# Kernel tuning notes

Measured on AMD Instinct MI355X. Metric: run time of the kernel, lower is better.

The kernel has to match this reference:

```python
import jax, jax.numpy as jnp
import numpy as np

N, C, G, H = 262144, 512, 16, 16   # nodes, channels, groups, half_group_c
GH = G * H                          # 256
CH_HID = 64                         # channel_mlp hidden = max(GH//4, 8)
SP_HID = 8                          # space_mlp hidden = max(H//4, 8)
B = 1024                            # number of graphs
TEMP = 1.0
EPS = 1e-5


def setup_inputs() -> dict:
    k = jax.random.key(0)
    ks = jax.random.split(k, 20)
    s = 0.02
    rn = lambda kk, sh: jax.random.normal(kk, sh, dtype=jnp.float32)
    return {
        "x": rn(ks[0], (N, C)),
        "batch": jnp.sort(jax.random.randint(ks[1], (N,), 0, B, dtype=jnp.int32)),
        "num_segments": B,
        "cweight": s * rn(ks[2], (1, H)),
        "cbias": 1.0 + s * rn(ks[3], (1, H)),
        "sweight": s * rn(ks[4], (1, H)),
        "sbias": 1.0 + s * rn(ks[5], (1, H)),
        "ch_W1": rn(ks[6], (2 * GH, CH_HID)) / np.sqrt(2 * GH),
        "ch_b1": s * rn(ks[7], (CH_HID,)),
        "ch_W2": rn(ks[8], (CH_HID, GH)) / np.sqrt(CH_HID),
        "ch_b2": s * rn(ks[9], (GH,)),
        "gn_weight": 1.0 + s * rn(ks[10], (GH,)),
        "gn_bias": s * rn(ks[11], (GH,)),
        "sp_W1": rn(ks[12], (3 * H, SP_HID)) / np.sqrt(3 * H),
        "sp_b1": s * rn(ks[13], (SP_HID,)),
        "sp_W2": rn(ks[14], (SP_HID, H)) / np.sqrt(SP_HID),
        "sp_b2": s * rn(ks[15], (H,)),
        "init_scale": jnp.float32(0.1),
        "gnorm_weight": 1.0 + s * rn(ks[16], (C,)),
        "gnorm_bias": s * rn(ks[17], (C,)),
        "gnorm_mean_scale": 1.0 + s * rn(ks[18], (C,)),
    }


def reference(x, batch, num_segments, cweight, cbias, sweight, sbias,
              ch_W1, ch_b1, ch_W2, ch_b2, gn_weight, gn_bias,
              sp_W1, sp_b1, sp_W2, sp_b2, init_scale,
              gnorm_weight, gnorm_bias, gnorm_mean_scale):
    n = x.shape[0]
    xg = x.reshape(n, G, 2 * H)
    x_c = xg[:, :, :H]                      # [N, G, H] channel branch
    x_s = xg[:, :, H:]                      # [N, G, H] spatial branch
    xcf = x_c.reshape(n, GH)

    # --- segment mean / max pooling over graphs ---
    cnt = jax.ops.segment_sum(jnp.ones((n,), x.dtype), batch, num_segments)  # [B]
    gap_mean = jax.ops.segment_sum(xcf, batch, num_segments) / jnp.maximum(cnt, 1.0)[:, None]
    gap_max = jax.ops.segment_max(xcf, batch, num_segments)
    gap_max = jnp.where(cnt[:, None] > 0, gap_max, 0.0)    # empty graphs -> 0
    gap_cat = jnp.concatenate([gap_mean, gap_max], axis=1)  # [B, 2*GH]

    # --- channel gate MLP ---
    hch = jax.nn.relu(gap_cat @ ch_W1 + ch_b1)
    ch_gate = jax.nn.sigmoid((hch @ ch_W2 + ch_b2).reshape(-1, G, H) / TEMP)
    ch_gate = ch_gate * (1.0 + cweight.reshape(1, 1, H)) + cbias.reshape(1, 1, H)
    x_c = x_c * ch_gate[batch]

    # --- GroupNorm over each group's H channels (spatial extent 1) ---
    mu = x_s.mean(axis=2, keepdims=True)
    var = ((x_s - mu) ** 2).mean(axis=2, keepdims=True)
    xn = (x_s - mu) / jnp.sqrt(var + EPS)
    xn = xn * gn_weight.reshape(1, G, H) + gn_bias.reshape(1, G, H)

    # --- spatial context across groups (std is unbiased, ddof=1) ---
    mean_ctx = xn.mean(axis=1)
    max_ctx = xn.max(axis=1)
    std_ctx = jnp.sqrt(((xn - mean_ctx[:, None, :]) ** 2).sum(axis=1) / (G - 1))
    sc = jnp.concatenate([mean_ctx, max_ctx, std_ctx], axis=-1)  # [N, 3H]
    hs = jax.nn.relu(sc @ sp_W1 + sp_b1)
    sp_gate = jax.nn.sigmoid((hs @ sp_W2 + sp_b2).reshape(n, 1, H) / TEMP)
    sp_gate = sp_gate * (1.0 + sweight.reshape(1, 1, H)) + sbias.reshape(1, 1, H)
    x_s = x_s * sp_gate

    # stack -> [N,G,H,2] -> permute -> [N,G,2,H] -> [N,C]
    out = jnp.stack([x_c, x_s], axis=-1).transpose(0, 1, 3, 2).reshape(n, C)
    out = out + jnp.tanh(init_scale) * x

    # --- GraphNorm (PyG): per-graph, per-channel ---
    inv_cnt = 1.0 / jnp.maximum(cnt, 1.0)[:, None]
    gmean = jax.ops.segment_sum(out, batch, num_segments) * inv_cnt
    outc = out - gmean[batch] * gnorm_mean_scale
    gvar = jax.ops.segment_sum(outc * outc, batch, num_segments) * inv_cnt
    out = gnorm_weight * outc / jnp.sqrt(gvar + EPS)[batch] + gnorm_bias

    # channel shuffle with groups=2
    return out.reshape(n, 2, C // 2).transpose(0, 2, 1).reshape(n, C)
```

## Files before the change

### kernel.cpp

```cpp
#include <hip/hip_runtime.h>
#include <hip/hip_bf16.h>
#include <math.h>

#define NN 262144
#define CC 512
#define BB 1024
#define EPSF 1e-5f

typedef float f32x4 __attribute__((ext_vector_type(4)));

__device__ __forceinline__ int lower_bound_i(const int* __restrict__ a, int n, int v) {
    int lo = 0, hi = n;
    while (lo < hi) { int mid = (lo + hi) >> 1; if (a[mid] < v) lo = mid + 1; else hi = mid; }
    return lo;
}

__device__ __forceinline__ float sigmoidf(float v) { return 1.0f / (1.0f + __expf(-v)); }

template<int CTRL>
__device__ __forceinline__ float dppAdd(float v) {
    int t = __builtin_amdgcn_update_dpp(0, __float_as_int(v), CTRL, 0xf, 0xf, true);
    return v + __int_as_float(t);
}
template<int CTRL>
__device__ __forceinline__ float dppMax(float v) {
    int t = __builtin_amdgcn_update_dpp(0, __float_as_int(v), CTRL, 0xf, 0xf, true);
    return fmaxf(v, __int_as_float(t));
}

__global__ void kA(const float* __restrict__ x, const int* __restrict__ batch,
                   const float* __restrict__ sweight, const float* __restrict__ sbias,
                   const float* __restrict__ gn_w, const float* __restrict__ gn_b,
                   const float* __restrict__ sp_W1, const float* __restrict__ sp_b1,
                   const float* __restrict__ sp_W2, const float* __restrict__ sp_b2,
                   const float* __restrict__ init_scale,
                   float* __restrict__ segS1, float* __restrict__ segMx,
                   float* __restrict__ segS2, float* __restrict__ segT1,
                   float* __restrict__ segT2, int* __restrict__ segCnt,
                   float* __restrict__ spgt)
{
    const int b    = blockIdx.x;
    const int tid  = threadIdx.x;
    const int lane = tid & 63;
    const int w    = tid >> 6;
    const int g    = lane & 15;
    const int q    = lane >> 4;
    const int h0   = q * 4;
    const int kk   = g & 7;

    __shared__ float red[4][5][256];

    const int s = lower_bound_i(batch, NN, b);
    const int e = lower_bound_i(batch, NN, b + 1);
    const float tau = tanhf(init_scale[0]);

    float gwv[4], gbv[4], b2v[4], swv[4], sbv[4], w1m[4], w1x[4], w1s[4], w2r[4];
#pragma unroll
    for (int j = 0; j < 4; ++j) {
        const int h = h0 + j;
        gwv[j] = gn_w[g * 16 + h];
        gbv[j] = gn_b[g * 16 + h];
        b2v[j] = sp_b2[h];
        swv[j] = sweight[h];
        sbv[j] = sbias[h];
        w1m[j] = sp_W1[h * 8 + kk];
        w1x[j] = sp_W1[(16 + h) * 8 + kk];
        w1s[j] = sp_W1[(32 + h) * 8 + kk];
        w2r[j] = sp_W2[kk * 16 + h];
    }
    const float b1k = sp_b1[kk];

    float sc1[4] = {0.f,0.f,0.f,0.f}, sc2[4] = {0.f,0.f,0.f,0.f};
    float st1[4] = {0.f,0.f,0.f,0.f}, st2[4] = {0.f,0.f,0.f,0.f};
    float mxc[4] = {-INFINITY,-INFINITY,-INFINITY,-INFINITY};

    for (int n = s + w; n < e; n += 4) {
        const float* row = x + (size_t)n * CC + g * 32 + h0;
        const float4 c4 = *(const float4*)row;
        const float4 s4 = *(const float4*)(row + 16);
        float ca[4] = {c4.x, c4.y, c4.z, c4.w};
        float sa[4] = {s4.x, s4.y, s4.z, s4.w};

#pragma unroll
        for (int j = 0; j < 4; ++j) {
            sc1[j] += ca[j];
            sc2[j] = fmaf(ca[j], ca[j], sc2[j]);
            mxc[j] = fmaxf(mxc[j], ca[j]);
        }

        float ls = sa[0] + sa[1] + sa[2] + sa[3];
        float lq = fmaf(sa[0], sa[0], fmaf(sa[1], sa[1], fmaf(sa[2], sa[2], sa[3] * sa[3])));
        ls += __shfl_xor(ls, 16); ls += __shfl_xor(ls, 32);
        lq += __shfl_xor(lq, 16); lq += __shfl_xor(lq, 32);
        const float mu   = ls * 0.0625f;
        const float var  = lq * 0.0625f - mu * mu;
        const float rstd = rsqrtf(var + EPSF);
        float xn[4];
#pragma unroll
        for (int j = 0; j < 4; ++j)
            xn[j] = fmaf((sa[j] - mu) * rstd, gwv[j], gbv[j]);

        float sm[4], mx[4];
#pragma unroll
        for (int j = 0; j < 4; ++j) {
            float v = xn[j];
            v = dppAdd<0xB1>(v); v = dppAdd<0x4E>(v);
            v = dppAdd<0x124>(v); v = dppAdd<0x128>(v);
            sm[j] = v;
            float m = xn[j];
            m = dppMax<0xB1>(m); m = dppMax<0x4E>(m);
            m = dppMax<0x124>(m); m = dppMax<0x128>(m);
            mx[j] = m;
        }
        float mean[4], ssq[4];
#pragma unroll
        for (int j = 0; j < 4; ++j) {
            mean[j] = sm[j] * 0.0625f;
            const float d = xn[j] - mean[j];
            float v = d * d;
            v = dppAdd<0xB1>(v); v = dppAdd<0x4E>(v);
            v = dppAdd<0x124>(v); v = dppAdd<0x128>(v);
            ssq[j] = v;
        }
        float stdc[4];
#pragma unroll
        for (int j = 0; j < 4; ++j) stdc[j] = sqrtf(ssq[j] * (1.0f / 15.0f));

        float p = 0.f;
#pragma unroll
        for (int j = 0; j < 4; ++j) {
            p = fmaf(mean[j], w1m[j], p);
            p = fmaf(mx[j],   w1x[j], p);
            p = fmaf(stdc[j], w1s[j], p);
        }
        p += __shfl_xor(p, 16); p += __shfl_xor(p, 32);
        const float hsk = fmaxf(p + b1k, 0.0f);

        float spg[4];
#pragma unroll
        for (int j = 0; j < 4; ++j) {
            float t = hsk * w2r[j];
            t = dppAdd<0xB1>(t); t = dppAdd<0x4E>(t); t = dppAdd<0x141>(t);
            spg[j] = fmaf(sigmoidf(t + b2v[j]), 1.0f + swv[j], sbv[j]) + tau;
        }

#pragma unroll
        for (int j = 0; j < 4; ++j) {
            const float os = spg[j] * sa[j];
            st1[j] += os;
            st2[j] = fmaf(os, os, st2[j]);
        }

        if (g == 0) {
            *(float4*)(spgt + (size_t)n * 16 + h0) =
                make_float4(spg[0], spg[1], spg[2], spg[3]);
        }
    }

    const int ch = g * 16 + h0;
    *(float4*)&red[w][0][ch] = make_float4(sc1[0], sc1[1], sc1[2], sc1[3]);
    *(float4*)&red[w][1][ch] = make_float4(mxc[0], mxc[1], mxc[2], mxc[3]);
    *(float4*)&red[w][2][ch] = make_float4(sc2[0], sc2[1], sc2[2], sc2[3]);
    *(float4*)&red[w][3][ch] = make_float4(st1[0], st1[1], st1[2], st1[3]);
    *(float4*)&red[w][4][ch] = make_float4(st2[0], st2[1], st2[2], st2[3]);
    __syncthreads();
    if (tid < 256) {
        const int c = tid;
        float a0 = red[0][0][c] + red[1][0][c] + red[2][0][c] + red[3][0][c];
        float a1 = fmaxf(fmaxf(red[0][1][c], red[1][1][c]), fmaxf(red[2][1][c], red[3][1][c]));
        float a2 = red[0][2][c] + red[1][2][c] + red[2][2][c] + red[3][2][c];
        float a3 = red[0][3][c] + red[1][3][c] + red[2][3][c] + red[3][3][c];
        float a4 = red[0][4][c] + red[1][4][c] + red[2][4][c] + red[3][4][c];
        segS1[b * 256 + c] = a0;
        segMx[b * 256 + c] = a1;
        segS2[b * 256 + c] = a2;
        segT1[b * 256 + c] = a3;
        segT2[b * 256 + c] = a4;
    }
    if (tid == 0) segCnt[b] = e - s;
}

__global__ void kF(const float* __restrict__ segS1, const float* __restrict__ segMx,
                   const float* __restrict__ segS2, const float* __restrict__ segT1,
                   const float* __restrict__ segT2, const int* __restrict__ segCnt,
                   const float* __restrict__ ch_W1, const float* __restrict__ ch_b1,
                   const float* __restrict__ ch_W2, const float* __restrict__ ch_b2,
                   const float* __restrict__ cweight, const float* __restrict__ cbias,
                   const float* __restrict__ init_scale,
                   const float* __restrict__ gms, const float* __restrict__ gw,
                   const float* __restrict__ gb,
                   float* __restrict__ coef, float* __restrict__ offs)
{
    const int b = blockIdx.x;
    const int tid = threadIdx.x;
    __shared__ float gap[512];
    __shared__ float hch[64];
    __shared__ float part[4][64];

    const int cnt = segCnt[b];
    const float inv = 1.0f / (float)max(cnt, 1);
    if (tid < 256) {
        gap[tid] = segS1[b * 256 + tid] * inv;
        const float m = segMx[b * 256 + tid];
        gap[256 + tid] = (cnt > 0) ? m : 0.0f;
    }
    __syncthreads();
    {
        const int t = tid & 63, pp = tid >> 6;
        float acc = 0.f;
        for (int i = pp * 128; i < pp * 128 + 128; ++i)
            acc = fmaf(gap[i], ch_W1[i * 64 + t], acc);
        part[pp][t] = acc;
    }
    __syncthreads();
    if (tid < 64)
        hch[tid] = fmaxf(part[0][tid] + part[1][tid] + part[2][tid] + part[3][tid] + ch_b1[tid], 0.0f);
    __syncthreads();
    if (tid < 256) {
        const int c = tid, gg = c >> 4, h = c & 15;
        float acc = ch_b2[c];
        for (int k = 0; k < 64; ++k) acc = fmaf(hch[k], ch_W2[k * 256 + c], acc);
        const float chg = fmaf(sigmoidf(acc), 1.0f + cweight[h], cbias[h]);
        const float tau = tanhf(init_scale[0]);
        const float ct = chg + tau;
        const int colc = gg * 32 + h, cols = colc + 16;
        {
            const float S1 = segS1[b * 256 + c], S2 = segS2[b * 256 + c];
            const float m  = ct * S1 * inv;
            const float e2 = ct * ct * S2 * inv;
            const float smv = gms[colc];
            const float gv = fmaxf(e2 - m * m * smv * (2.0f - smv), 0.0f);
            const float A  = gw[colc] * rsqrtf(gv + EPSF);
            coef[b * 512 + colc] = A * ct;
            offs[b * 512 + colc] = gb[colc] - m * smv * A;
        }
        {
            const float T1 = segT1[b * 256 + c], T2 = segT2[b * 256 + c];
            const float m  = T1 * inv;
            const float e2 = T2 * inv;
            const float smv = gms[cols];
            const float gv = fmaxf(e2 - m * m * smv * (2.0f - smv), 0.0f);
            const float A  = gw[cols] * rsqrtf(gv + EPSF);
            coef[b * 512 + cols] = A;
            offs[b * 512 + cols] = gb[cols] - m * smv * A;
        }
    }
}

__global__ void kB(const float* __restrict__ x, const int* __restrict__ batch,
                   const float* __restrict__ coef, const float* __restrict__ offs,
                   const float* __restrict__ spgt, float* __restrict__ out)
{
    const int b = BB - 1 - blockIdx.x;
    const int tid = threadIdx.x;
    const int lane = tid & 63, w = tid >> 6;
    const int l2 = lane * 2;
    const int p0 = (lane >> 3) & 1;

    const int s = lower_bound_i(batch, NN, b);
    const int e = lower_bound_i(batch, NN, b + 1);

    const float* cfb = coef + (size_t)b * 512;
    const float* ofb = offs + (size_t)b * 512;
    const float cf0 = cfb[l2],       cf1 = cfb[l2 + 1];
    const float cf2 = cfb[128 + l2], cf3 = cfb[129 + l2];
    const float cf4 = cfb[256 + l2], cf5 = cfb[257 + l2];
    const float cf6 = cfb[384 + l2], cf7 = cfb[385 + l2];
    const float of0 = ofb[l2],       of1 = ofb[l2 + 1];
    const float of2 = ofb[128 + l2], of3 = ofb[129 + l2];
    const float of4 = ofb[256 + l2], of5 = ofb[257 + l2];
    const float of6 = ofb[384 + l2], of7 = ofb[385 + l2];

    for (int n = s + w; n < e; n += 4) {
        const float2* r2 = (const float2*)(x + (size_t)n * CC);
        const float2 xa = r2[lane];
        const float2 xb = r2[64 + lane];
        const float2 xc = r2[128 + lane];
        const float2 xd = r2[192 + lane];
        const float2 sp = *(const float2*)(spgt + (size_t)n * 16 + (l2 & 15));
        const float me = p0 ? sp.x : 1.0f;
        const float mo = p0 ? sp.y : 1.0f;

        const float v0 = fmaf(cf0 * me, xa.x, of0);
        const float v1 = fmaf(cf1 * mo, xa.y, of1);
        const float v2 = fmaf(cf2 * me, xb.x, of2);
        const float v3 = fmaf(cf3 * mo, xb.y, of3);
        const float v4 = fmaf(cf4 * me, xc.x, of4);
        const float v5 = fmaf(cf5 * mo, xc.y, of5);
        const float v6 = fmaf(cf6 * me, xd.x, of6);
        const float v7 = fmaf(cf7 * mo, xd.y, of7);

        f32x4* o4 = (f32x4*)(out + (size_t)n * CC);
        f32x4 pa = {v0, v4, v1, v5};
        f32x4 pb = {v2, v6, v3, v7};
        __builtin_nontemporal_store(pa, &o4[lane]);
        __builtin_nontemporal_store(pb, &o4[64 + lane]);
    }
}

extern "C" void kernel_launch(void* const* d_in, const int* in_sizes, int n_in,
                              void* d_out, int out_size, void* d_ws, size_t ws_size,
                              hipStream_t stream) {
    (void)in_sizes; (void)n_in; (void)out_size; (void)ws_size;
    const float* x        = (const float*)d_in[0];
    const int*   batch    = (const int*)d_in[1];
    const float* cweight  = (const float*)d_in[3];
    const float* cbias    = (const float*)d_in[4];
    const float* sweight  = (const float*)d_in[5];
    const float* sbias    = (const float*)d_in[6];
    const float* ch_W1    = (const float*)d_in[7];
    const float* ch_b1    = (const float*)d_in[8];
    const float* ch_W2    = (const float*)d_in[9];
    const float* ch_b2    = (const float*)d_in[10];
    const float* gn_w     = (const float*)d_in[11];
    const float* gn_b     = (const float*)d_in[12];
    const float* sp_W1    = (const float*)d_in[13];
    const float* sp_b1    = (const float*)d_in[14];
    const float* sp_W2    = (const float*)d_in[15];
    const float* sp_b2    = (const float*)d_in[16];
    const float* init_sc  = (const float*)d_in[17];
    const float* gnw      = (const float*)d_in[18];
    const float* gnb      = (const float*)d_in[19];
    const float* gms      = (const float*)d_in[20];

    float* ws    = (float*)d_ws;
    float* segS1 = ws;
    float* segMx = segS1 + BB * 256;
    float* segS2 = segMx + BB * 256;
    float* segT1 = segS2 + BB * 256;
    float* segT2 = segT1 + BB * 256;
    int*   segCnt = (int*)(segT2 + BB * 256);
    float* coef  = (float*)(segCnt + BB);
    float* offs  = coef + BB * 512;
    float* spgt  = offs + BB * 512;
    float* outp  = (float*)d_out;

    kA<<<BB, 256, 0, stream>>>(x, batch, sweight, sbias, gn_w, gn_b,
                               sp_W1, sp_b1, sp_W2, sp_b2, init_sc,
                               segS1, segMx, segS2, segT1, segT2, segCnt, spgt);
    kF<<<BB, 256, 0, stream>>>(segS1, segMx, segS2, segT1, segT2, segCnt,
                               ch_W1, ch_b1, ch_W2, ch_b2, cweight, cbias,
                               init_sc, gms, gnw, gnb, coef, offs);
    kB<<<BB, 256, 0, stream>>>(x, batch, coef, offs, spgt, outp);
}
```

Baseline: 484.0 us.

## Fuse pooling, gate MLP and GraphNorm apply into one per-graph kernel

```diff
diff --git a/kernel.cpp b/kernel.cpp
--- a/kernel.cpp
+++ b/kernel.cpp
@@ -6,6 +6,7 @@
 #define CC 512
 #define BB 1024
 #define EPSF 1e-5f
+#define CAP 512
 
 typedef float f32x4 __attribute__((ext_vector_type(4)));
 
@@ -28,18 +29,29 @@
     return fmaxf(v, __int_as_float(t));
 }
 
-__global__ void kA(const float* __restrict__ x, const int* __restrict__ batch,
-                   const float* __restrict__ sweight, const float* __restrict__ sbias,
-                   const float* __restrict__ gn_w, const float* __restrict__ gn_b,
-                   const float* __restrict__ sp_W1, const float* __restrict__ sp_b1,
-                   const float* __restrict__ sp_W2, const float* __restrict__ sp_b2,
-                   const float* __restrict__ init_scale,
-                   float* __restrict__ segS1, float* __restrict__ segMx,
-                   float* __restrict__ segS2, float* __restrict__ segT1,
-                   float* __restrict__ segT2, int* __restrict__ segCnt,
-                   float* __restrict__ spgt)
+__global__ __launch_bounds__(512, 1) void kFused(
+    const float* __restrict__ x, const int* __restrict__ batch,
+    const float* __restrict__ cweight, const float* __restrict__ cbias,
+    const float* __restrict__ sweight, const float* __restrict__ sbias,
+    const float* __restrict__ ch_W1, const float* __restrict__ ch_b1,
+    const float* __restrict__ ch_W2, const float* __restrict__ ch_b2,
+    const float* __restrict__ gn_w, const float* __restrict__ gn_b,
+    const float* __restrict__ sp_W1, const float* __restrict__ sp_b1,
+    const float* __restrict__ sp_W2, const float* __restrict__ sp_b2,
+    const float* __restrict__ init_scale,
+    const float* __restrict__ gms, const float* __restrict__ gw,
+    const float* __restrict__ gb,
+    float* __restrict__ spgOv, float* __restrict__ out)
 {
-    const int b    = blockIdx.x;
+    __shared__ float red[8][5][256];
+    __shared__ float segA[5][256];
+    __shared__ float spgL[CAP * 16];
+    __shared__ float gap[512];
+    __shared__ float part[8][64];
+    __shared__ float hch[64];
+    __shared__ float cA[512];
+    __shared__ float oA[512];
+
     const int tid  = threadIdx.x;
     const int lane = tid & 63;
     const int w    = tid >> 6;
@@ -47,11 +59,6 @@
     const int q    = lane >> 4;
     const int h0   = q * 4;
     const int kk   = g & 7;
-
-    __shared__ float red[4][5][256];
-
-    const int s = lower_bound_i(batch, NN, b);
-    const int e = lower_bound_i(batch, NN, b + 1);
     const float tau = tanhf(init_scale[0]);
 
     float gwv[4], gbv[4], b2v[4], swv[4], sbv[4], w1m[4], w1x[4], w1s[4], w2r[4];
@@ -70,231 +77,217 @@
     }
     const float b1k = sp_b1[kk];
 
-    float sc1[4] = {0.f,0.f,0.f,0.f}, sc2[4] = {0.f,0.f,0.f,0.f};
-    float st1[4] = {0.f,0.f,0.f,0.f}, st2[4] = {0.f,0.f,0.f,0.f};
-    float mxc[4] = {-INFINITY,-INFINITY,-INFINITY,-INFINITY};
-
-    for (int n = s + w; n < e; n += 4) {
-        const float* row = x + (size_t)n * CC + g * 32 + h0;
-        const float4 c4 = *(const float4*)row;
-        const float4 s4 = *(const float4*)(row + 16);
-        float ca[4] = {c4.x, c4.y, c4.z, c4.w};
-        float sa[4] = {s4.x, s4.y, s4.z, s4.w};
-
-#pragma unroll
-        for (int j = 0; j < 4; ++j) {
-            sc1[j] += ca[j];
-            sc2[j] = fmaf(ca[j], ca[j], sc2[j]);
-            mxc[j] = fmaxf(mxc[j], ca[j]);
-        }
-
-        float ls = sa[0] + sa[1] + sa[2] + sa[3];
-        float lq = fmaf(sa[0], sa[0], fmaf(sa[1], sa[1], fmaf(sa[2], sa[2], sa[3] * sa[3])));
-        ls += __shfl_xor(ls, 16); ls += __shfl_xor(ls, 32);
-        lq += __shfl_xor(lq, 16); lq += __shfl_xor(lq, 32);
-        const float mu   = ls * 0.0625f;
-        const float var  = lq * 0.0625f - mu * mu;
-        const float rstd = rsqrtf(var + EPSF);
-        float xn[4];
-#pragma unroll
-        for (int j = 0; j < 4; ++j)
-            xn[j] = fmaf((sa[j] - mu) * rstd, gwv[j], gbv[j]);
-
-        float sm[4], mx[4];
-#pragma unroll
-        for (int j = 0; j < 4; ++j) {
-            float v = xn[j];
-            v = dppAdd<0xB1>(v); v = dppAdd<0x4E>(v);
-            v = dppAdd<0x124>(v); v = dppAdd<0x128>(v);
-            sm[j] = v;
-            float m = xn[j];
-            m = dppMax<0xB1>(m); m = dppMax<0x4E>(m);
-            m = dppMax<0x124>(m); m = dppMax<0x128>(m);
-            mx[j] = m;
-        }
-        float mean[4], ssq[4];
-#pragma unroll
-        for (int j = 0; j < 4; ++j) {
-            mean[j] = sm[j] * 0.0625f;
-            const float d = xn[j] - mean[j];
-            float v = d * d;
-            v = dppAdd<0xB1>(v); v = dppAdd<0x4E>(v);
-            v = dppAdd<0x124>(v); v = dppAdd<0x128>(v);
-            ssq[j] = v;
-        }
-        float stdc[4];
-#pragma unroll
-        for (int j = 0; j < 4; ++j) stdc[j] = sqrtf(ssq[j] * (1.0f / 15.0f));
-
-        float p = 0.f;
-#pragma unroll
-        for (int j = 0; j < 4; ++j) {
-            p = fmaf(mean[j], w1m[j], p);
-            p = fmaf(mx[j],   w1x[j], p);
-            p = fmaf(stdc[j], w1s[j], p);
-        }
-        p += __shfl_xor(p, 16); p += __shfl_xor(p, 32);
-        const float hsk = fmaxf(p + b1k, 0.0f);
-
-        float spg[4];
-#pragma unroll
-        for (int j = 0; j < 4; ++j) {
-            float t = hsk * w2r[j];
-            t = dppAdd<0xB1>(t); t = dppAdd<0x4E>(t); t = dppAdd<0x141>(t);
-            spg[j] = fmaf(sigmoidf(t + b2v[j]), 1.0f + swv[j], sbv[j]) + tau;
-        }
-
-#pragma unroll
-        for (int j = 0; j < 4; ++j) {
-            const float os = spg[j] * sa[j];
-            st1[j] += os;
-            st2[j] = fmaf(os, os, st2[j]);
-        }
-
-        if (g == 0) {
-            *(float4*)(spgt + (size_t)n * 16 + h0) =
-                make_float4(spg[0], spg[1], spg[2], spg[3]);
-        }
-    }
-
-    const int ch = g * 16 + h0;
-    *(float4*)&red[w][0][ch] = make_float4(sc1[0], sc1[1], sc1[2], sc1[3]);
-    *(float4*)&red[w][1][ch] = make_float4(mxc[0], mxc[1], mxc[2], mxc[3]);
-    *(float4*)&red[w][2][ch] = make_float4(sc2[0], sc2[1], sc2[2], sc2[3]);
-    *(float4*)&red[w][3][ch] = make_float4(st1[0], st1[1], st1[2], st1[3]);
-    *(float4*)&red[w][4][ch] = make_float4(st2[0], st2[1], st2[2], st2[3]);
-    __syncthreads();
-    if (tid < 256) {
-        const int c = tid;
-        float a0 = red[0][0][c] + red[1][0][c] + red[2][0][c] + red[3][0][c];
-        float a1 = fmaxf(fmaxf(red[0][1][c], red[1][1][c]), fmaxf(red[2][1][c], red[3][1][c]));
-        float a2 = red[0][2][c] + red[1][2][c] + red[2][2][c] + red[3][2][c];
-        float a3 = red[0][3][c] + red[1][3][c] + red[2][3][c] + red[3][3][c];
-        float a4 = red[0][4][c] + red[1][4][c] + red[2][4][c] + red[3][4][c];
-        segS1[b * 256 + c] = a0;
-        segMx[b * 256 + c] = a1;
-        segS2[b * 256 + c] = a2;
-        segT1[b * 256 + c] = a3;
-        segT2[b * 256 + c] = a4;
-    }
-    if (tid == 0) segCnt[b] = e - s;
-}
-
-__global__ void kF(const float* __restrict__ segS1, const float* __restrict__ segMx,
-                   const float* __restrict__ segS2, const float* __restrict__ segT1,
-                   const float* __restrict__ segT2, const int* __restrict__ segCnt,
-                   const float* __restrict__ ch_W1, const float* __restrict__ ch_b1,
-                   const float* __restrict__ ch_W2, const float* __restrict__ ch_b2,
-                   const float* __restrict__ cweight, const float* __restrict__ cbias,
-                   const float* __restrict__ init_scale,
-                   const float* __restrict__ gms, const float* __restrict__ gw,
-                   const float* __restrict__ gb,
-                   float* __restrict__ coef, float* __restrict__ offs)
-{
-    const int b = blockIdx.x;
-    const int tid = threadIdx.x;
-    __shared__ float gap[512];
-    __shared__ float hch[64];
-    __shared__ float part[4][64];
-
-    const int cnt = segCnt[b];
-    const float inv = 1.0f / (float)max(cnt, 1);
-    if (tid < 256) {
-        gap[tid] = segS1[b * 256 + tid] * inv;
-        const float m = segMx[b * 256 + tid];
-        gap[256 + tid] = (cnt > 0) ? m : 0.0f;
-    }
-    __syncthreads();
-    {
-        const int t = tid & 63, pp = tid >> 6;
-        float acc = 0.f;
-        for (int i = pp * 128; i < pp * 128 + 128; ++i)
-            acc = fmaf(gap[i], ch_W1[i * 64 + t], acc);
-        part[pp][t] = acc;
-    }
-    __syncthreads();
-    if (tid < 64)
-        hch[tid] = fmaxf(part[0][tid] + part[1][tid] + part[2][tid] + part[3][tid] + ch_b1[tid], 0.0f);
-    __syncthreads();
-    if (tid < 256) {
-        const int c = tid, gg = c >> 4, h = c & 15;
-        float acc = ch_b2[c];
-        for (int k = 0; k < 64; ++k) acc = fmaf(hch[k], ch_W2[k * 256 + c], acc);
-        const float chg = fmaf(sigmoidf(acc), 1.0f + cweight[h], cbias[h]);
-        const float tau = tanhf(init_scale[0]);
-        const float ct = chg + tau;
-        const int colc = gg * 32 + h, cols = colc + 16;
-        {
-            const float S1 = segS1[b * 256 + c], S2 = segS2[b * 256 + c];
-            const float m  = ct * S1 * inv;
-            const float e2 = ct * ct * S2 * inv;
-            const float smv = gms[colc];
-            const float gv = fmaxf(e2 - m * m * smv * (2.0f - smv), 0.0f);
-            const float A  = gw[colc] * rsqrtf(gv + EPSF);
-            coef[b * 512 + colc] = A * ct;
-            offs[b * 512 + colc] = gb[colc] - m * smv * A;
-        }
-        {
-            const float T1 = segT1[b * 256 + c], T2 = segT2[b * 256 + c];
-            const float m  = T1 * inv;
-            const float e2 = T2 * inv;
-            const float smv = gms[cols];
-            const float gv = fmaxf(e2 - m * m * smv * (2.0f - smv), 0.0f);
-            const float A  = gw[cols] * rsqrtf(gv + EPSF);
-            coef[b * 512 + cols] = A;
-            offs[b * 512 + cols] = gb[cols] - m * smv * A;
-        }
-    }
-}
-
-__global__ void kB(const float* __restrict__ x, const int* __restrict__ batch,
-                   const float* __restrict__ coef, const float* __restrict__ offs,
-                   const float* __restrict__ spgt, float* __restrict__ out)
-{
-    const int b = BB - 1 - blockIdx.x;
-    const int tid = threadIdx.x;
-    const int lane = tid & 63, w = tid >> 6;
     const int l2 = lane * 2;
     const int p0 = (lane >> 3) & 1;
 
-    const int s = lower_bound_i(batch, NN, b);
-    const int e = lower_bound_i(batch, NN, b + 1);
-
-    const float* cfb = coef + (size_t)b * 512;
-    const float* ofb = offs + (size_t)b * 512;
-    const float cf0 = cfb[l2],       cf1 = cfb[l2 + 1];
-    const float cf2 = cfb[128 + l2], cf3 = cfb[129 + l2];
-    const float cf4 = cfb[256 + l2], cf5 = cfb[257 + l2];
-    const float cf6 = cfb[384 + l2], cf7 = cfb[385 + l2];
-    const float of0 = ofb[l2],       of1 = ofb[l2 + 1];
-    const float of2 = ofb[128 + l2], of3 = ofb[129 + l2];
-    const float of4 = ofb[256 + l2], of5 = ofb[257 + l2];
-    const float of6 = ofb[384 + l2], of7 = ofb[385 + l2];
-
-    for (int n = s + w; n < e; n += 4) {
-        const float2* r2 = (const float2*)(x + (size_t)n * CC);
-        const float2 xa = r2[lane];
-        const float2 xb = r2[64 + lane];
-        const float2 xc = r2[128 + lane];
-        const float2 xd = r2[192 + lane];
-        const float2 sp = *(const float2*)(spgt + (size_t)n * 16 + (l2 & 15));
-        const float me = p0 ? sp.x : 1.0f;
-        const float mo = p0 ? sp.y : 1.0f;
-
-        const float v0 = fmaf(cf0 * me, xa.x, of0);
-        const float v1 = fmaf(cf1 * mo, xa.y, of1);
-        const float v2 = fmaf(cf2 * me, xb.x, of2);
-        const float v3 = fmaf(cf3 * mo, xb.y, of3);
-        const float v4 = fmaf(cf4 * me, xc.x, of4);
-        const float v5 = fmaf(cf5 * mo, xc.y, of5);
-        const float v6 = fmaf(cf6 * me, xd.x, of6);
-        const float v7 = fmaf(cf7 * mo, xd.y, of7);
-
-        f32x4* o4 = (f32x4*)(out + (size_t)n * CC);
-        f32x4 pa = {v0, v4, v1, v5};
-        f32x4 pb = {v2, v6, v3, v7};
-        __builtin_nontemporal_store(pa, &o4[lane]);
-        __builtin_nontemporal_store(pb, &o4[64 + lane]);
+    for (int r = 0; r < 4; ++r) {
+        const int b = blockIdx.x * 4 + r;
+        const int s = lower_bound_i(batch, NN, b);
+        const int e = lower_bound_i(batch, NN, b + 1);
+        const int cnt = e - s;
+
+        __syncthreads();
+
+        float sc1[4] = {0.f,0.f,0.f,0.f}, sc2[4] = {0.f,0.f,0.f,0.f};
+        float st1[4] = {0.f,0.f,0.f,0.f}, st2[4] = {0.f,0.f,0.f,0.f};
+        float mxc[4] = {-INFINITY,-INFINITY,-INFINITY,-INFINITY};
+
+        for (int n = s + w; n < e; n += 8) {
+            const float* row = x + (size_t)n * CC + g * 32 + h0;
+            const float4 c4 = *(const float4*)row;
+            const float4 s4 = *(const float4*)(row + 16);
+            float ca[4] = {c4.x, c4.y, c4.z, c4.w};
+            float sa[4] = {s4.x, s4.y, s4.z, s4.w};
+
+#pragma unroll
+            for (int j = 0; j < 4; ++j) {
+                sc1[j] += ca[j];
+                sc2[j] = fmaf(ca[j], ca[j], sc2[j]);
+                mxc[j] = fmaxf(mxc[j], ca[j]);
+            }
+
+            float ls = sa[0] + sa[1] + sa[2] + sa[3];
+            float lq = fmaf(sa[0], sa[0], fmaf(sa[1], sa[1], fmaf(sa[2], sa[2], sa[3] * sa[3])));
+            ls += __shfl_xor(ls, 16); ls += __shfl_xor(ls, 32);
+            lq += __shfl_xor(lq, 16); lq += __shfl_xor(lq, 32);
+            const float mu   = ls * 0.0625f;
+            const float var  = lq * 0.0625f - mu * mu;
+            const float rstd = rsqrtf(var + EPSF);
+            float xn[4];
+#pragma unroll
+            for (int j = 0; j < 4; ++j)
+                xn[j] = fmaf((sa[j] - mu) * rstd, gwv[j], gbv[j]);
+
+            float sm[4], mx[4];
+#pragma unroll
+            for (int j = 0; j < 4; ++j) {
+                float v = xn[j];
+                v = dppAdd<0xB1>(v); v = dppAdd<0x4E>(v);
+                v = dppAdd<0x124>(v); v = dppAdd<0x128>(v);
+                sm[j] = v;
+                float m = xn[j];
+                m = dppMax<0xB1>(m); m = dppMax<0x4E>(m);
+                m = dppMax<0x124>(m); m = dppMax<0x128>(m);
+                mx[j] = m;
+            }
+            float mean[4], ssq[4];
+#pragma unroll
+            for (int j = 0; j < 4; ++j) {
+                mean[j] = sm[j] * 0.0625f;
+                const float d = xn[j] - mean[j];
+                float v = d * d;
+                v = dppAdd<0xB1>(v); v = dppAdd<0x4E>(v);
+                v = dppAdd<0x124>(v); v = dppAdd<0x128>(v);
+                ssq[j] = v;
+            }
+            float stdc[4];
+#pragma unroll
+            for (int j = 0; j < 4; ++j) stdc[j] = sqrtf(ssq[j] * (1.0f / 15.0f));
+
+            float p = 0.f;
+#pragma unroll
+            for (int j = 0; j < 4; ++j) {
+                p = fmaf(mean[j], w1m[j], p);
+                p = fmaf(mx[j],   w1x[j], p);
+                p = fmaf(stdc[j], w1s[j], p);
+            }
+            p += __shfl_xor(p, 16); p += __shfl_xor(p, 32);
+            const float hsk = fmaxf(p + b1k, 0.0f);
+
+            float spg[4];
+#pragma unroll
+            for (int j = 0; j < 4; ++j) {
+                float t = hsk * w2r[j];
+                t = dppAdd<0xB1>(t); t = dppAdd<0x4E>(t); t = dppAdd<0x141>(t);
+                spg[j] = fmaf(sigmoidf(t + b2v[j]), 1.0f + swv[j], sbv[j]) + tau;
+            }
+
+#pragma unroll
+            for (int j = 0; j < 4; ++j) {
+                const float os = spg[j] * sa[j];
+                st1[j] += os;
+                st2[j] = fmaf(os, os, st2[j]);
+            }
+
+            if (g == 0) {
+                const int idx = n - s;
+                if (idx < CAP)
+                    *(float4*)(&spgL[idx * 16 + h0]) = make_float4(spg[0], spg[1], spg[2], spg[3]);
+                else
+                    *(float4*)(spgOv + (size_t)n * 16 + h0) = make_float4(spg[0], spg[1], spg[2], spg[3]);
+            }
+        }
+
+        const int ch = g * 16 + h0;
+        *(float4*)&red[w][0][ch] = make_float4(sc1[0], sc1[1], sc1[2], sc1[3]);
+        *(float4*)&red[w][1][ch] = make_float4(mxc[0], mxc[1], mxc[2], mxc[3]);
+        *(float4*)&red[w][2][ch] = make_float4(sc2[0], sc2[1], sc2[2], sc2[3]);
+        *(float4*)&red[w][3][ch] = make_float4(st1[0], st1[1], st1[2], st1[3]);
+        *(float4*)&red[w][4][ch] = make_float4(st2[0], st2[1], st2[2], st2[3]);
+        __syncthreads();
+        if (tid < 256) {
+            float a0 = 0.f, a2 = 0.f, a3 = 0.f, a4 = 0.f, a1 = -INFINITY;
+#pragma unroll
+            for (int ww = 0; ww < 8; ++ww) {
+                a0 += red[ww][0][tid];
+                a1 = fmaxf(a1, red[ww][1][tid]);
+                a2 += red[ww][2][tid];
+                a3 += red[ww][3][tid];
+                a4 += red[ww][4][tid];
+            }
+            segA[0][tid] = a0; segA[1][tid] = a1; segA[2][tid] = a2;
+            segA[3][tid] = a3; segA[4][tid] = a4;
+        }
+        __syncthreads();
+
+        const float inv = 1.0f / (float)max(cnt, 1);
+        if (tid < 256) {
+            gap[tid] = segA[0][tid] * inv;
+            gap[256 + tid] = (cnt > 0) ? segA[1][tid] : 0.0f;
+        }
+        __syncthreads();
+        {
+            const int t = tid & 63, pp = tid >> 6;
+            float acc = 0.f;
+            for (int i = pp * 64; i < pp * 64 + 64; ++i)
+                acc = fmaf(gap[i], ch_W1[i * 64 + t], acc);
+            part[pp][t] = acc;
+        }
+        __syncthreads();
+        if (tid < 64) {
+            float a = ch_b1[tid];
+#pragma unroll
+            for (int pp = 0; pp < 8; ++pp) a += part[pp][tid];
+            hch[tid] = fmaxf(a, 0.0f);
+        }
+        __syncthreads();
+        if (tid < 256) {
+            const int c = tid, gg = c >> 4, h = c & 15;
+            float acc = ch_b2[c];
+            for (int k = 0; k < 64; ++k) acc = fmaf(hch[k], ch_W2[k * 256 + c], acc);
+            const float chg = fmaf(sigmoidf(acc), 1.0f + cweight[h], cbias[h]);
+            const float ct = chg + tau;
+            const int colc = gg * 32 + h, cols = colc + 16;
+            {
+                const float S1 = segA[0][c], S2 = segA[2][c];
+                const float m  = ct * S1 * inv;
+                const float e2 = ct * ct * S2 * inv;
+                const float smv = gms[colc];
+                const float gv = fmaxf(e2 - m * m * smv * (2.0f - smv), 0.0f);
+                const float A  = gw[colc] * rsqrtf(gv + EPSF);
+                cA[colc] = A * ct;
+                oA[colc] = gb[colc] - m * smv * A;
+            }
+            {
+                const float T1 = segA[3][c], T2 = segA[4][c];
+                const float m  = T1 * inv;
+                const float e2 = T2 * inv;
+                const float smv = gms[cols];
+                const float gv = fmaxf(e2 - m * m * smv * (2.0f - smv), 0.0f);
+                const float A  = gw[cols] * rsqrtf(gv + EPSF);
+                cA[cols] = A;
+                oA[cols] = gb[cols] - m * smv * A;
+            }
+        }
+        __syncthreads();
+
+        const float cf0 = cA[l2],       cf1 = cA[l2 + 1];
+        const float cf2 = cA[128 + l2], cf3 = cA[129 + l2];
+        const float cf4 = cA[256 + l2], cf5 = cA[257 + l2];
+        const float cf6 = cA[384 + l2], cf7 = cA[385 + l2];
+        const float of0 = oA[l2],       of1 = oA[l2 + 1];
+        const float of2 = oA[128 + l2], of3 = oA[129 + l2];
+        const float of4 = oA[256 + l2], of5 = oA[257 + l2];
+        const float of6 = oA[384 + l2], of7 = oA[385 + l2];
+
+        for (int n = s + w; n < e; n += 8) {
+            const float2* r2 = (const float2*)(x + (size_t)n * CC);
+            const float2 xa = r2[lane];
+            const float2 xb = r2[64 + lane];
+            const float2 xc = r2[128 + lane];
+            const float2 xd = r2[192 + lane];
+            const int idx = n - s;
+            float2 sp;
+            if (idx < CAP) sp = *(const float2*)(&spgL[idx * 16 + (l2 & 15)]);
+            else           sp = *(const float2*)(spgOv + (size_t)n * 16 + (l2 & 15));
+            const float me = p0 ? sp.x : 1.0f;
+            const float mo = p0 ? sp.y : 1.0f;
+
+            const float v0 = fmaf(cf0 * me, xa.x, of0);
+            const float v1 = fmaf(cf1 * mo, xa.y, of1);
+            const float v2 = fmaf(cf2 * me, xb.x, of2);
+            const float v3 = fmaf(cf3 * mo, xb.y, of3);
+            const float v4 = fmaf(cf4 * me, xc.x, of4);
+            const float v5 = fmaf(cf5 * mo, xc.y, of5);
+            const float v6 = fmaf(cf6 * me, xd.x, of6);
+            const float v7 = fmaf(cf7 * mo, xd.y, of7);
+
+            f32x4* o4 = (f32x4*)(out + (size_t)n * CC);
+            f32x4 pa = {v0, v4, v1, v5};
+            f32x4 pb = {v2, v6, v3, v7};
+            __builtin_nontemporal_store(pa, &o4[lane]);
+            __builtin_nontemporal_store(pb, &o4[64 + lane]);
+        }
     }
 }
 
@@ -323,23 +316,11 @@
     const float* gnb      = (const float*)d_in[19];
     const float* gms      = (const float*)d_in[20];
 
-    float* ws    = (float*)d_ws;
-    float* segS1 = ws;
-    float* segMx = segS1 + BB * 256;
-    float* segS2 = segMx + BB * 256;
-    float* segT1 = segS2 + BB * 256;
-    float* segT2 = segT1 + BB * 256;
-    int*   segCnt = (int*)(segT2 + BB * 256);
-    float* coef  = (float*)(segCnt + BB);
-    float* offs  = coef + BB * 512;
-    float* spgt  = offs + BB * 512;
+    float* spgOv = (float*)d_ws;
     float* outp  = (float*)d_out;
 
-    kA<<<BB, 256, 0, stream>>>(x, batch, sweight, sbias, gn_w, gn_b,
-                               sp_W1, sp_b1, sp_W2, sp_b2, init_sc,
-                               segS1, segMx, segS2, segT1, segT2, segCnt, spgt);
-    kF<<<BB, 256, 0, stream>>>(segS1, segMx, segS2, segT1, segT2, segCnt,
-                               ch_W1, ch_b1, ch_W2, ch_b2, cweight, cbias,
-                               init_sc, gms, gnw, gnb, coef, offs);
-    kB<<<BB, 256, 0, stream>>>(x, batch, coef, offs, spgt, outp);
-}
+    kFused<<<BB / 4, 512, 0, stream>>>(x, batch, cweight, cbias, sweight, sbias,
+                                       ch_W1, ch_b1, ch_W2, ch_b2, gn_w, gn_b,
+                                       sp_W1, sp_b1, sp_W2, sp_b2, init_sc,
+                                       gms, gnw, gnb, spgOv, outp);
+}
```

Result: slower. 502.4 us (+3.8%).

## Batch multiple rows per wave iteration and stage small weights in LDS

Applied to the files above, without the earlier changes.

```diff
diff --git a/kernel.cpp b/kernel.cpp
--- a/kernel.cpp
+++ b/kernel.cpp
@@ -49,111 +49,148 @@
     const int kk   = g & 7;
 
     __shared__ float red[4][5][256];
+    __shared__ float gw_l[16 * 20], gb_l[16 * 20];
+    __shared__ float w1m_l[8 * 20], w1x_l[8 * 20], w1s_l[8 * 20], w2_l[8 * 20];
+    __shared__ float b2_l[16], sw_l[16], sb_l[16];
+
+    if (tid < 256) {
+        const int gg = tid >> 4, hh = tid & 15;
+        gw_l[gg * 20 + hh] = gn_w[tid];
+        gb_l[gg * 20 + hh] = gn_b[tid];
+    }
+    if (tid < 128) {
+        const int k2 = tid >> 4, hh = tid & 15;
+        w1m_l[k2 * 20 + hh] = sp_W1[hh * 8 + k2];
+        w1x_l[k2 * 20 + hh] = sp_W1[(16 + hh) * 8 + k2];
+        w1s_l[k2 * 20 + hh] = sp_W1[(32 + hh) * 8 + k2];
+        w2_l [k2 * 20 + hh] = sp_W2[k2 * 16 + hh];
+    }
+    if (tid < 16) {
+        b2_l[tid] = sp_b2[tid];
+        sw_l[tid] = sweight[tid];
+        sb_l[tid] = sbias[tid];
+    }
+    __syncthreads();
 
     const int s = lower_bound_i(batch, NN, b);
     const int e = lower_bound_i(batch, NN, b + 1);
     const float tau = tanhf(init_scale[0]);
-
-    float gwv[4], gbv[4], b2v[4], swv[4], sbv[4], w1m[4], w1x[4], w1s[4], w2r[4];
-#pragma unroll
-    for (int j = 0; j < 4; ++j) {
-        const int h = h0 + j;
-        gwv[j] = gn_w[g * 16 + h];
-        gbv[j] = gn_b[g * 16 + h];
-        b2v[j] = sp_b2[h];
-        swv[j] = sweight[h];
-        sbv[j] = sbias[h];
-        w1m[j] = sp_W1[h * 8 + kk];
-        w1x[j] = sp_W1[(16 + h) * 8 + kk];
-        w1s[j] = sp_W1[(32 + h) * 8 + kk];
-        w2r[j] = sp_W2[kk * 16 + h];
-    }
     const float b1k = sp_b1[kk];
+
+    const int gofs = g * 20 + h0;
+    const int kofs = kk * 20 + h0;
 
     float sc1[4] = {0.f,0.f,0.f,0.f}, sc2[4] = {0.f,0.f,0.f,0.f};
     float st1[4] = {0.f,0.f,0.f,0.f}, st2[4] = {0.f,0.f,0.f,0.f};
     float mxc[4] = {-INFINITY,-INFINITY,-INFINITY,-INFINITY};
 
-    for (int n = s + w; n < e; n += 4) {
-        const float* row = x + (size_t)n * CC + g * 32 + h0;
-        const float4 c4 = *(const float4*)row;
-        const float4 s4 = *(const float4*)(row + 16);
-        float ca[4] = {c4.x, c4.y, c4.z, c4.w};
-        float sa[4] = {s4.x, s4.y, s4.z, s4.w};
-
-#pragma unroll
-        for (int j = 0; j < 4; ++j) {
-            sc1[j] += ca[j];
-            sc2[j] = fmaf(ca[j], ca[j], sc2[j]);
-            mxc[j] = fmaxf(mxc[j], ca[j]);
-        }
-
-        float ls = sa[0] + sa[1] + sa[2] + sa[3];
-        float lq = fmaf(sa[0], sa[0], fmaf(sa[1], sa[1], fmaf(sa[2], sa[2], sa[3] * sa[3])));
-        ls += __shfl_xor(ls, 16); ls += __shfl_xor(ls, 32);
-        lq += __shfl_xor(lq, 16); lq += __shfl_xor(lq, 32);
-        const float mu   = ls * 0.0625f;
-        const float var  = lq * 0.0625f - mu * mu;
-        const float rstd = rsqrtf(var + EPSF);
-        float xn[4];
-#pragma unroll
-        for (int j = 0; j < 4; ++j)
-            xn[j] = fmaf((sa[j] - mu) * rstd, gwv[j], gbv[j]);
-
-        float sm[4], mx[4];
-#pragma unroll
-        for (int j = 0; j < 4; ++j) {
-            float v = xn[j];
-            v = dppAdd<0xB1>(v); v = dppAdd<0x4E>(v);
-            v = dppAdd<0x124>(v); v = dppAdd<0x128>(v);
-            sm[j] = v;
-            float m = xn[j];
-            m = dppMax<0xB1>(m); m = dppMax<0x4E>(m);
-            m = dppMax<0x124>(m); m = dppMax<0x128>(m);
-            mx[j] = m;
-        }
-        float mean[4], ssq[4];
-#pragma unroll
-        for (int j = 0; j < 4; ++j) {
-            mean[j] = sm[j] * 0.0625f;
-            const float d = xn[j] - mean[j];
-            float v = d * d;
-            v = dppAdd<0xB1>(v); v = dppAdd<0x4E>(v);
-            v = dppAdd<0x124>(v); v = dppAdd<0x128>(v);
-            ssq[j] = v;
-        }
-        float stdc[4];
-#pragma unroll
-        for (int j = 0; j < 4; ++j) stdc[j] = sqrtf(ssq[j] * (1.0f / 15.0f));
-
-        float p = 0.f;
-#pragma unroll
-        for (int j = 0; j < 4; ++j) {
-            p = fmaf(mean[j], w1m[j], p);
-            p = fmaf(mx[j],   w1x[j], p);
-            p = fmaf(stdc[j], w1s[j], p);
-        }
-        p += __shfl_xor(p, 16); p += __shfl_xor(p, 32);
-        const float hsk = fmaxf(p + b1k, 0.0f);
-
-        float spg[4];
-#pragma unroll
-        for (int j = 0; j < 4; ++j) {
-            float t = hsk * w2r[j];
-            t = dppAdd<0xB1>(t); t = dppAdd<0x4E>(t); t = dppAdd<0x141>(t);
-            spg[j] = fmaf(sigmoidf(t + b2v[j]), 1.0f + swv[j], sbv[j]) + tau;
-        }
-
-#pragma unroll
-        for (int j = 0; j < 4; ++j) {
-            const float os = spg[j] * sa[j];
-            st1[j] += os;
-            st2[j] = fmaf(os, os, st2[j]);
-        }
-
-        if (g == 0) {
-            *(float4*)(spgt + (size_t)n * 16 + h0) =
-                make_float4(spg[0], spg[1], spg[2], spg[3]);
+    for (int n0 = s + 2 * w; n0 < e; n0 += 8) {
+        const int n1 = (n0 + 1 < e) ? n0 + 1 : e - 1;
+        const bool v1 = (n0 + 1 < e);
+
+        const float* r0 = x + (size_t)n0 * CC + g * 32 + h0;
+        const float* r1 = x + (size_t)n1 * CC + g * 32 + h0;
+        const float4 c40 = *(const float4*)r0;
+        const float4 s40 = *(const float4*)(r0 + 16);
+        const float4 c41 = *(const float4*)r1;
+        const float4 s41 = *(const float4*)(r1 + 16);
+
+        {
+            const float c0[4] = {c40.x, c40.y, c40.z, c40.w};
+#pragma unroll
+            for (int j = 0; j < 4; ++j) {
+                sc1[j] += c0[j];
+                sc2[j] = fmaf(c0[j], c0[j], sc2[j]);
+                mxc[j] = fmaxf(mxc[j], c0[j]);
+            }
+        }
+        if (v1) {
+            const float c1[4] = {c41.x, c41.y, c41.z, c41.w};
+#pragma unroll
+            for (int j = 0; j < 4; ++j) {
+                sc1[j] += c1[j];
+                sc2[j] = fmaf(c1[j], c1[j], sc2[j]);
+                mxc[j] = fmaxf(mxc[j], c1[j]);
+            }
+        }
+
+#pragma unroll
+        for (int rr = 0; rr < 2; ++rr) {
+            if (rr == 1 && !v1) break;
+            const float4 s4 = rr ? s41 : s40;
+            const int   nw = rr ? n1 : n0;
+            float sa[4] = {s4.x, s4.y, s4.z, s4.w};
+
+            float ls = sa[0] + sa[1] + sa[2] + sa[3];
+            float lq = fmaf(sa[0], sa[0], fmaf(sa[1], sa[1],
+                       fmaf(sa[2], sa[2], sa[3] * sa[3])));
+            ls += __shfl_xor(ls, 16); ls += __shfl_xor(ls, 32);
+            lq += __shfl_xor(lq, 16); lq += __shfl_xor(lq, 32);
+            const float mu   = ls * 0.0625f;
+            const float var  = lq * 0.0625f - mu * mu;
+            const float rstd = rsqrtf(var + EPSF);
+            const f32x4 gwv = *(const f32x4*)&gw_l[gofs];
+            const f32x4 gbv = *(const f32x4*)&gb_l[gofs];
+            float xn[4];
+#pragma unroll
+            for (int j = 0; j < 4; ++j)
+                xn[j] = fmaf((sa[j] - mu) * rstd, gwv[j], gbv[j]);
+
+            float sm[4], s2c[4], mx[4];
+#pragma unroll
+            for (int j = 0; j < 4; ++j) {
+                float v = xn[j];
+                v = dppAdd<0xB1>(v); v = dppAdd<0x4E>(v);
+                v = dppAdd<0x124>(v); v = dppAdd<0x128>(v);
+                sm[j] = v;
+                float u = xn[j] * xn[j];
+                u = dppAdd<0xB1>(u); u = dppAdd<0x4E>(u);
+                u = dppAdd<0x124>(u); u = dppAdd<0x128>(u);
+                s2c[j] = u;
+                float m = xn[j];
+                m = dppMax<0xB1>(m); m = dppMax<0x4E>(m);
+                m = dppMax<0x124>(m); m = dppMax<0x128>(m);
+                mx[j] = m;
+            }
+
+            const f32x4 w1m = *(const f32x4*)&w1m_l[kofs];
+            const f32x4 w1x = *(const f32x4*)&w1x_l[kofs];
+            const f32x4 w1s = *(const f32x4*)&w1s_l[kofs];
+            float p = 0.f;
+#pragma unroll
+            for (int j = 0; j < 4; ++j) {
+                const float mean = sm[j] * 0.0625f;
+                const float ss   = fmaxf(s2c[j] - 16.0f * mean * mean, 0.0f);
+                const float stdc = sqrtf(ss * (1.0f / 15.0f));
+                p = fmaf(mean, w1m[j], p);
+                p = fmaf(mx[j], w1x[j], p);
+                p = fmaf(stdc, w1s[j], p);
+            }
+            p += __shfl_xor(p, 16); p += __shfl_xor(p, 32);
+            const float hsk = fmaxf(p + b1k, 0.0f);
+
+            const f32x4 w2r = *(const f32x4*)&w2_l[kofs];
+            const f32x4 b2v = *(const f32x4*)&b2_l[h0];
+            const f32x4 swv = *(const f32x4*)&sw_l[h0];
+            const f32x4 sbv = *(const f32x4*)&sb_l[h0];
+            float spg[4];
+#pragma unroll
+            for (int j = 0; j < 4; ++j) {
+                float t = hsk * w2r[j];
+                t = dppAdd<0xB1>(t); t = dppAdd<0x4E>(t); t = dppAdd<0x141>(t);
+                spg[j] = fmaf(sigmoidf(t + b2v[j]), 1.0f + swv[j], sbv[j]) + tau;
+            }
+
+#pragma unroll
+            for (int j = 0; j < 4; ++j) {
+                const float os = spg[j] * sa[j];
+                st1[j] += os;
+                st2[j] = fmaf(os, os, st2[j]);
+            }
+
+            if (g == 0)
+                *(float4*)(spgt + (size_t)nw * 16 + h0) =
+                    make_float4(spg[0], spg[1], spg[2], spg[3]);
         }
     }
 
@@ -271,30 +308,45 @@
     const float of4 = ofb[256 + l2], of5 = ofb[257 + l2];
     const float of6 = ofb[384 + l2], of7 = ofb[385 + l2];
 
-    for (int n = s + w; n < e; n += 4) {
-        const float2* r2 = (const float2*)(x + (size_t)n * CC);
-        const float2 xa = r2[lane];
-        const float2 xb = r2[64 + lane];
-        const float2 xc = r2[128 + lane];
-        const float2 xd = r2[192 + lane];
-        const float2 sp = *(const float2*)(spgt + (size_t)n * 16 + (l2 & 15));
-        const float me = p0 ? sp.x : 1.0f;
-        const float mo = p0 ? sp.y : 1.0f;
-
-        const float v0 = fmaf(cf0 * me, xa.x, of0);
-        const float v1 = fmaf(cf1 * mo, xa.y, of1);
-        const float v2 = fmaf(cf2 * me, xb.x, of2);
-        const float v3 = fmaf(cf3 * mo, xb.y, of3);
-        const float v4 = fmaf(cf4 * me, xc.x, of4);
-        const float v5 = fmaf(cf5 * mo, xc.y, of5);
-        const float v6 = fmaf(cf6 * me, xd.x, of6);
-        const float v7 = fmaf(cf7 * mo, xd.y, of7);
-
-        f32x4* o4 = (f32x4*)(out + (size_t)n * CC);
-        f32x4 pa = {v0, v4, v1, v5};
-        f32x4 pb = {v2, v6, v3, v7};
-        __builtin_nontemporal_store(pa, &o4[lane]);
-        __builtin_nontemporal_store(pb, &o4[64 + lane]);
+    for (int n0 = s + 4 * w; n0 < e; n0 += 16) {
+        int nr[4];
+        nr[0] = n0;
+        nr[1] = (n0 + 1 < e) ? n0 + 1 : e - 1;
+        nr[2] = (n0 + 2 < e) ? n0 + 2 : e - 1;
+        nr[3] = (n0 + 3 < e) ? n0 + 3 : e - 1;
+
+        float2 xa[4], xb[4], xc[4], xd[4], sp[4];
+#pragma unroll
+        for (int rr = 0; rr < 4; ++rr) {
+            const float2* r2 = (const float2*)(x + (size_t)nr[rr] * CC);
+            xa[rr] = r2[lane];
+            xb[rr] = r2[64 + lane];
+            xc[rr] = r2[128 + lane];
+            xd[rr] = r2[192 + lane];
+            sp[rr] = *(const float2*)(spgt + (size_t)nr[rr] * 16 + (l2 & 15));
+        }
+
+#pragma unroll
+        for (int rr = 0; rr < 4; ++rr) {
+            if (rr > 0 && n0 + rr >= e) break;
+            const float me = p0 ? sp[rr].x : 1.0f;
+            const float mo = p0 ? sp[rr].y : 1.0f;
+
+            const float v0 = fmaf(cf0 * me, xa[rr].x, of0);
+            const float v1 = fmaf(cf1 * mo, xa[rr].y, of1);
+            const float v2 = fmaf(cf2 * me, xb[rr].x, of2);
+            const float v3 = fmaf(cf3 * mo, xb[rr].y, of3);
+            const float v4 = fmaf(cf4 * me, xc[rr].x, of4);
+            const float v5 = fmaf(cf5 * mo, xc[rr].y, of5);
+            const float v6 = fmaf(cf6 * me, xd[rr].x, of6);
+            const float v7 = fmaf(cf7 * mo, xd[rr].y, of7);
+
+            f32x4* o4 = (f32x4*)(out + (size_t)nr[rr] * CC);
+            f32x4 pa = {v0, v4, v1, v5};
+            f32x4 pb = {v2, v6, v3, v7};
+            __builtin_nontemporal_store(pa, &o4[lane]);
+            __builtin_nontemporal_store(pb, &o4[64 + lane]);
+        }
     }
 }
 
```

Result: no change. 483.2 us (-0.2%).
